# Performance work log

Measured on AMD Instinct MI355X. Metric: run time of the kernel, lower is better.

The kernel has to match this reference:

```python
import jax, jax.numpy as jnp
import numpy as np

B, P, ENC = 128, 196, 2048
D, A, ED, V, L = 512, 512, 512, 10000, 20


def setup_inputs() -> dict:
    key = jax.random.key(0)
    ks = jax.random.split(key, 24)
    s = 0.02
    inp = {
        'encoder_out': jax.random.normal(ks[0], (B, P, ENC), jnp.float32),
        'captions': jax.random.randint(ks[1], (B, L), 0, V),
        'caption_len': jax.random.randint(ks[2], (B,), 2, L + 1).at[0].set(L),
        # embedding (uniform(-0.1, 0.1) per init_weights)
        'emb_w': jax.random.uniform(ks[3], (V, ED), jnp.float32, -0.1, 0.1),
        # LSTMCell: input = ED + ENC, hidden = D, gates order i,f,g,o
        'Wih': jax.random.normal(ks[4], (4 * D, ED + ENC), jnp.float32) * s,
        'Whh': jax.random.normal(ks[5], (4 * D, D), jnp.float32) * s,
        'bih': jax.random.normal(ks[6], (4 * D,), jnp.float32) * s,
        'bhh': jax.random.normal(ks[7], (4 * D,), jnp.float32) * s,
        # init hidden state projections
        'h0_w': jax.random.normal(ks[8], (D, ENC), jnp.float32) * s,
        'h0_b': jnp.zeros((D,), jnp.float32),
        'c0_w': jax.random.normal(ks[9], (D, ENC), jnp.float32) * s,
        'c0_b': jnp.zeros((D,), jnp.float32),
        # gate D -> ENC
        'gate_w': jax.random.normal(ks[10], (ENC, D), jnp.float32) * s,
        'gate_b': jnp.zeros((ENC,), jnp.float32),
        # output projection D -> V (uniform(-0.1,0.1), bias 0 per init_weights)
        'lin_w': jax.random.uniform(ks[11], (V, D), jnp.float32, -0.1, 0.1),
        'lin_b': jnp.zeros((V,), jnp.float32),
        # attention network
        'ea_w': jax.random.normal(ks[12], (A, ENC), jnp.float32) * s,
        'ea_b': jnp.zeros((A,), jnp.float32),
        'da_w': jax.random.normal(ks[13], (A, D), jnp.float32) * s,
        'da_b': jnp.zeros((A,), jnp.float32),
        'fa_w': jax.random.normal(ks[14], (1, A), jnp.float32) * s,
        'fa_b': jnp.zeros((1,), jnp.float32),
    }
    return inp


def reference(encoder_out, captions, caption_len, emb_w, Wih, Whh, bih, bhh,
              h0_w, h0_b, c0_w, c0_b, gate_w, gate_b, lin_w, lin_b,
              ea_w, ea_b, da_w, da_b, fa_w, fa_b):
    # sort by caption length descending (as in torch .sort(descending=True))
    order = jnp.argsort(-caption_len)
    cap_len = caption_len[order]
    enc = encoder_out[order]            # [B, P, ENC]
    caps = captions[order]              # [B, L]
    dec_len = cap_len - 1               # per-example decode lengths

    emb = emb_w[caps]                   # [B, L, ED]
    mean_enc = enc.mean(axis=1)         # [B, ENC]
    h0 = mean_enc @ h0_w.T + h0_b       # [B, D]
    c0 = mean_enc @ c0_w.T + c0_b
    att1 = enc @ ea_w.T + ea_b          # [B, P, A] precomputed encoder attention

    T = caps.shape[1] - 1               # static max decode steps (caption_len[0]=L)

    def step(carry, i):
        h, c = carry
        # Bahdanau attention
        att2 = h @ da_w.T + da_b                                   # [B, A]
        e = (jax.nn.relu(att1 + att2[:, None, :]) @ fa_w.T + fa_b)[..., 0]  # [B, P]
        alpha = jax.nn.softmax(e, axis=1)
        awe = jnp.einsum('bp,bpe->be', alpha, enc)                 # [B, ENC]
        g = jax.nn.sigmoid(h @ gate_w.T + gate_b)
        awe = g * awe
        # LSTMCell
        x = jnp.concatenate([emb[:, i, :], awe], axis=1)           # [B, ED+ENC]
        gates = x @ Wih.T + bih + h @ Whh.T + bhh                  # [B, 4D]
        gi, gf, gg, go = jnp.split(gates, 4, axis=1)
        c_new = jax.nn.sigmoid(gf) * c + jax.nn.sigmoid(gi) * jnp.tanh(gg)
        h_new = jax.nn.sigmoid(go) * jnp.tanh(c_new)
        active = (i < dec_len)[:, None]                            # ragged mask
        # inactive rows keep old state (matches h[:batch_size_i] slicing)
        h2 = jnp.where(active, h_new, h)
        c2 = jnp.where(active, c_new, c)
        # dropout is identity in eval; output projection masked to zeros
        pred = jnp.where(active, h_new @ lin_w.T + lin_b, 0.0)     # [B, V]
        alpha = jnp.where(active, alpha, 0.0)
        return (h2, c2), (pred, alpha)

    (_, _), (preds, alphas) = jax.lax.scan(step, (h0, c0), jnp.arange(T))
    pred = jnp.swapaxes(preds, 0, 1)     # [B, T, V]
    alphas = jnp.swapaxes(alphas, 0, 1)  # [B, T, P]
    return pred, caps, dec_len, alphas, order
```

## Files before the change

kernel.cpp:

```cpp
#include <hip/hip_runtime.h>
#include <hip/hip_bf16.h>
#include <math.h>

#define Bn 128
#define Pn 196
#define ENCn 2048
#define Dn 512
#define An 512
#define EDn 512
#define Vn 10000
#define Ln 20
#define Tn 19

typedef short v8s __attribute__((ext_vector_type(8)));
typedef float v4f __attribute__((ext_vector_type(4)));

__device__ __forceinline__ float sigf(float x){ return 1.f/(1.f+__expf(-x)); }
__device__ __forceinline__ unsigned short f2bf(float f){
  unsigned u = __float_as_uint(f);
  return (unsigned short)((u + 0x7FFFu + ((u>>16)&1u)) >> 16);
}
__device__ __forceinline__ float bf2f(unsigned short h){
  return __uint_as_float(((unsigned)h)<<16);
}


__global__ void k_order(const int* __restrict__ caption_len,
                        const int* __restrict__ captions,
                        int* __restrict__ order_i, int* __restrict__ declen_i,
                        int* __restrict__ caps_s,
                        float* __restrict__ out_caps, float* __restrict__ out_declen,
                        float* __restrict__ out_order)
{
  __shared__ int lens[Bn];
  int b = threadIdx.x;
  lens[b] = caption_len[b];
  __syncthreads();
  int lb = lens[b];
  int r = 0;
  for (int j = 0; j < Bn; ++j) {
    int lj = lens[j];
    r += (int)((lj > lb) || (lj == lb && j < b));
  }
  order_i[r] = b;
  declen_i[r] = lb - 1;
  out_order[r] = (float)b;
  out_declen[r] = (float)(lb - 1);
  for (int t = 0; t < Ln; ++t) {
    int cv = captions[b*Ln + t];
    caps_s[r*Ln + t] = cv;
    out_caps[r*Ln + t] = (float)cv;
  }
}

__global__ void k_setup_bias(const float* __restrict__ bih, const float* __restrict__ bhh,
                             const float* __restrict__ da_b, const float* __restrict__ gate_b,
                             const float* __restrict__ h0_b, const float* __restrict__ c0_b,
                             float* __restrict__ bsum_r, float* __restrict__ dg_b,
                             float* __restrict__ hc_b)
{
  int i = blockIdx.x*256 + threadIdx.x;
  if (i < 2048) {
    int d = i >> 2, g = i & 3;
    bsum_r[i] = bih[g*512+d] + bhh[g*512+d];
  }
  if (i < 2560) dg_b[i] = (i < 512) ? da_b[i] : gate_b[i-512];
  if (i < 1024) hc_b[i] = (i < 512) ? h0_b[i] : c0_b[i-512];
}

__global__ void k_cvt(const float* __restrict__ src, unsigned short* __restrict__ dst, int n)
{
  int i = (blockIdx.x*256 + threadIdx.x)*4;
  if (i < n) {
    float4 v = *(const float4*)(src + i);
    dst[i+0]=f2bf(v.x); dst[i+1]=f2bf(v.y); dst[i+2]=f2bf(v.z); dst[i+3]=f2bf(v.w);
  }
}

__global__ void k_wcat(const float* __restrict__ Wih, const float* __restrict__ Whh,
                       unsigned short* __restrict__ dst)
{
  int i = (blockIdx.x*256 + threadIdx.x)*4;
  if (i >= 2048*3072) return;
  int rp = i/3072, j = i - rp*3072;
  int d = rp >> 2, g = rp & 3;
  int r = g*512 + d;
  const float* s = (j < 2560) ? (Wih + (size_t)r*2560 + j) : (Whh + (size_t)r*512 + (j-2560));
  float4 v = *(const float4*)s;
  dst[i+0]=f2bf(v.x); dst[i+1]=f2bf(v.y); dst[i+2]=f2bf(v.z); dst[i+3]=f2bf(v.w);
}

__global__ void k_cvt_enc(const float* __restrict__ enc, const int* __restrict__ order_i,
                          unsigned short* __restrict__ dst)
{
  int id = blockIdx.x;
  int b = id / Pn, p = id - b*Pn;
  const float* src = enc + ((size_t)order_i[b]*Pn + p)*ENCn;
  unsigned short* d = dst + (size_t)id*ENCn;
  int i = threadIdx.x*8;
  float4 v0 = *(const float4*)(src+i), v1 = *(const float4*)(src+i+4);
  d[i+0]=f2bf(v0.x); d[i+1]=f2bf(v0.y); d[i+2]=f2bf(v0.z); d[i+3]=f2bf(v0.w);
  d[i+4]=f2bf(v1.x); d[i+5]=f2bf(v1.y); d[i+6]=f2bf(v1.z); d[i+7]=f2bf(v1.w);
}

__global__ void k_mean(const unsigned short* __restrict__ enc_bf,
                       unsigned short* __restrict__ mean_bf)
{
  int b = blockIdx.x;
  const unsigned short* eb = enc_bf + (size_t)b*Pn*ENCn;
  for (int e = threadIdx.x; e < ENCn; e += 256) {
    float s = 0.f;
    for (int p = 0; p < Pn; ++p) s += bf2f(eb[(size_t)p*ENCn + e]);
    mean_bf[b*ENCn + e] = f2bf(s * (1.f/196.f));
  }
}

__global__ void k_zero(uint4* __restrict__ p, int n)
{
  int i = blockIdx.x*256 + threadIdx.x;
  if (i < n) p[i] = uint4{0,0,0,0};
}

__global__ void k_emb_all(const int* __restrict__ caps_s, const float* __restrict__ emb_w,
                          unsigned short* __restrict__ xh_all)
{
  int id = blockIdx.x; int t = id >> 7, b = id & 127;
  int tok = caps_s[b*Ln + t];
  const float* src = emb_w + (size_t)tok*EDn;
  unsigned short* d = xh_all + ((size_t)t*Bn + b)*3072;
  int i = threadIdx.x*2;
  float2 v = *(const float2*)(src+i);
  d[i] = f2bf(v.x); d[i+1] = f2bf(v.y);
}

__global__ void k_h2bf(const float* __restrict__ hc, float* __restrict__ c,
                       unsigned short* __restrict__ h_bf, unsigned short* __restrict__ xh_all)
{
  int b = blockIdx.x, d = threadIdx.x;
  float hv = hc[b*1024 + d];
  float cv = hc[b*1024 + 512 + d];
  c[b*Dn + d] = cv;
  unsigned short hb = f2bf(hv);
  h_bf[b*Dn + d] = hb;
  xh_all[(size_t)b*3072 + 2560 + d] = hb;
}

__global__ __launch_bounds__(256) void k_mfma_gemm(
    const unsigned short* __restrict__ Aw, const unsigned short* __restrict__ Bw,
    const float* __restrict__ bias, float* __restrict__ Cp,
    int N, int K, size_t ldc,
    const int* __restrict__ actlen, int t)
{
  __shared__ unsigned short smA[2][4096];
  __shared__ unsigned short smB[2][4096];
  const int tid = threadIdx.x;
  const int bm0 = blockIdx.y*64, bn0 = blockIdx.x*64;
  if (actlen && actlen[bm0] <= t) return;

  const int lane = tid & 63, w = tid >> 6;
  const int wr = w >> 1, wc = w & 1;
  const int lrow = lane & 15, kq = lane >> 4;

  v4f acc[2][2];
  #pragma unroll
  for (int i=0;i<2;++i)
    #pragma unroll
    for (int j=0;j<2;++j) acc[i][j] = (v4f)0.f;

  const int nt = K >> 6;

  auto stage = [&](int buf, int k0) {
    #pragma unroll
    for (int it = 0; it < 2; ++it) {
      int s = it*256 + tid;
      int row = s >> 3;
      int kb  = (s & 7) ^ (row & 7);
      *(v8s*)&smA[buf][s*8] = *(const v8s*)(Aw + (size_t)(bm0+row)*K + k0 + kb*8);
      *(v8s*)&smB[buf][s*8] = *(const v8s*)(Bw + (size_t)(bn0+row)*K + k0 + kb*8);
    }
  };
  auto compute = [&](int buf) {
    #pragma unroll
    for (int kc = 0; kc < 2; ++kc) {
      v8s aF[2], bF[2];
      #pragma unroll
      for (int mi = 0; mi < 2; ++mi) {
        int row = wr*32 + mi*16 + lrow;
        int kb = kc*4 + kq;
        aF[mi] = *(const v8s*)&smA[buf][row*64 + ((kb ^ (row&7))<<3)];
      }
      #pragma unroll
      for (int ni = 0; ni < 2; ++ni) {
        int row = wc*32 + ni*16 + lrow;
        int kb = kc*4 + kq;
        bF[ni] = *(const v8s*)&smB[buf][row*64 + ((kb ^ (row&7))<<3)];
      }
      #pragma unroll
      for (int mi = 0; mi < 2; ++mi)
        #pragma unroll
        for (int ni = 0; ni < 2; ++ni)
          acc[mi][ni] = __builtin_amdgcn_mfma_f32_16x16x32_bf16(aF[mi], bF[ni], acc[mi][ni], 0, 0, 0);
    }
  };

  stage(0, 0);
  __syncthreads();
  for (int tk = 0; tk < nt; ++tk) {
    if (tk + 1 < nt) stage((tk+1)&1, (tk+1)<<6);
    compute(tk&1);
    __syncthreads();
  }

  #pragma unroll
  for (int mi=0; mi<2; ++mi)
    #pragma unroll
    for (int ni=0; ni<2; ++ni)
      #pragma unroll
      for (int r=0; r<4; ++r) {
        int m = bm0 + wr*32 + mi*16 + kq*4 + r;
        int n = bn0 + wc*32 + ni*16 + lrow;
        Cp[(size_t)m*ldc + n] = acc[mi][ni][r] + bias[n];
      }
}

__global__ __launch_bounds__(256) void k_att1(
    const unsigned short* __restrict__ Aw, const unsigned short* __restrict__ Bw,
    const float* __restrict__ bias, unsigned short* __restrict__ Cp)
{
  __shared__ unsigned short smA[2][8192];
  __shared__ unsigned short smB[2][4096];
  const int tid = threadIdx.x;
  const int id = blockIdx.x;
  const int g = (id & 7)*196 + (id >> 3);
  const int bm0 = (g >> 3) * 128, bn0 = (g & 7) * 64;
  const int K = ENCn;

  const int lane = tid & 63, w = tid >> 6;
  const int wr = w >> 1, wc = w & 1;
  const int lrow = lane & 15, kq = lane >> 4;

  v4f acc[4][2];
  #pragma unroll
  for (int i=0;i<4;++i)
    #pragma unroll
    for (int j=0;j<2;++j) acc[i][j] = (v4f)0.f;

  auto stage = [&](int buf, int k0) {
    #pragma unroll
    for (int it = 0; it < 4; ++it) {
      int s = it*256 + tid;
      int row = s >> 3;
      int kb  = (s & 7) ^ (row & 7);
      *(v8s*)&smA[buf][s*8] = *(const v8s*)(Aw + (size_t)(bm0+row)*K + k0 + kb*8);
    }
    #pragma unroll
    for (int it = 0; it < 2; ++it) {
      int s = it*256 + tid;
      int row = s >> 3;
      int kb  = (s & 7) ^ (row & 7);
      *(v8s*)&smB[buf][s*8] = *(const v8s*)(Bw + (size_t)(bn0+row)*K + k0 + kb*8);
    }
  };
  auto compute = [&](int buf) {
    #pragma unroll
    for (int kc = 0; kc < 2; ++kc) {
      v8s aF[4], bF[2];
      #pragma unroll
      for (int mi = 0; mi < 4; ++mi) {
        int row = wr*64 + mi*16 + lrow;
        int kb = kc*4 + kq;
        aF[mi] = *(const v8s*)&smA[buf][row*64 + ((kb ^ (row&7))<<3)];
      }
      #pragma unroll
      for (int ni = 0; ni < 2; ++ni) {
        int row = wc*32 + ni*16 + lrow;
        int kb = kc*4 + kq;
        bF[ni] = *(const v8s*)&smB[buf][row*64 + ((kb ^ (row&7))<<3)];
      }
      #pragma unroll
      for (int mi = 0; mi < 4; ++mi)
        #pragma unroll
        for (int ni = 0; ni < 2; ++ni)
          acc[mi][ni] = __builtin_amdgcn_mfma_f32_16x16x32_bf16(aF[mi], bF[ni], acc[mi][ni], 0, 0, 0);
    }
  };

  stage(0, 0);
  __syncthreads();
  const int nt = K >> 6;
  for (int tk = 0; tk < nt; ++tk) {
    if (tk + 1 < nt) stage((tk+1)&1, (tk+1)<<6);
    compute(tk&1);
    __syncthreads();
  }

  #pragma unroll
  for (int mi=0; mi<4; ++mi)
    #pragma unroll
    for (int ni=0; ni<2; ++ni)
      #pragma unroll
      for (int r=0; r<4; ++r) {
        int m = bm0 + wr*64 + mi*16 + kq*4 + r;
        int n = bn0 + wc*32 + ni*16 + lrow;
        Cp[(size_t)m*An + n] = f2bf(acc[mi][ni][r] + bias[n]);
      }
}

__global__ __launch_bounds__(256) void k_gates_lstm(
    const unsigned short* __restrict__ Aw, const unsigned short* __restrict__ Bw,
    const float* __restrict__ bias,
    float* __restrict__ c, unsigned short* __restrict__ h_bf,
    unsigned short* __restrict__ h_all, unsigned short* __restrict__ xh_all,
    const int* __restrict__ declen_i, int t)
{
  __shared__ unsigned short smA[2][4096];
  __shared__ unsigned short smB[2][4096];
  __shared__ float smC[64][65];
  const int tid = threadIdx.x;
  const int bm0 = blockIdx.y*64, bn0 = blockIdx.x*64;
  if (declen_i[bm0] <= t) return;

  const int lane = tid & 63, w = tid >> 6;
  const int wr = w >> 1, wc = w & 1;
  const int lrow = lane & 15, kq = lane >> 4;
  const int K = 3072;

  v4f acc[2][2];
  #pragma unroll
  for (int i=0;i<2;++i)
    #pragma unroll
    for (int j=0;j<2;++j) acc[i][j] = (v4f)0.f;

  auto stage = [&](int buf, int k0) {
    #pragma unroll
    for (int it = 0; it < 2; ++it) {
      int s = it*256 + tid;
      int row = s >> 3;
      int kb  = (s & 7) ^ (row & 7);
      *(v8s*)&smA[buf][s*8] = *(const v8s*)(Aw + (size_t)(bm0+row)*K + k0 + kb*8);
      *(v8s*)&smB[buf][s*8] = *(const v8s*)(Bw + (size_t)(bn0+row)*K + k0 + kb*8);
    }
  };
  auto compute = [&](int buf) {
    #pragma unroll
    for (int kc = 0; kc < 2; ++kc) {
      v8s aF[2], bF[2];
      #pragma unroll
      for (int mi = 0; mi < 2; ++mi) {
        int row = wr*32 + mi*16 + lrow;
        int kb = kc*4 + kq;
        aF[mi] = *(const v8s*)&smA[buf][row*64 + ((kb ^ (row&7))<<3)];
      }
      #pragma unroll
      for (int ni = 0; ni < 2; ++ni) {
        int row = wc*32 + ni*16 + lrow;
        int kb = kc*4 + kq;
        bF[ni] = *(const v8s*)&smB[buf][row*64 + ((kb ^ (row&7))<<3)];
      }
      #pragma unroll
      for (int mi = 0; mi < 2; ++mi)
        #pragma unroll
        for (int ni = 0; ni < 2; ++ni)
          acc[mi][ni] = __builtin_amdgcn_mfma_f32_16x16x32_bf16(aF[mi], bF[ni], acc[mi][ni], 0, 0, 0);
    }
  };

  stage(0, 0);
  __syncthreads();
  const int nt = K >> 6;
  for (int tk = 0; tk < nt; ++tk) {
    if (tk + 1 < nt) stage((tk+1)&1, (tk+1)<<6);
    compute(tk&1);
    __syncthreads();
  }

  #pragma unroll
  for (int mi=0; mi<2; ++mi)
    #pragma unroll
    for (int ni=0; ni<2; ++ni)
      #pragma unroll
      for (int r=0; r<4; ++r) {
        int ml = wr*32 + mi*16 + kq*4 + r;
        int nl = wc*32 + ni*16 + lrow;
        smC[ml][nl] = acc[mi][ni][r] + bias[bn0 + nl];
      }
  __syncthreads();

  for (int idx = tid; idx < 1024; idx += 256) {
    int ml = idx >> 4, dl = idx & 15;
    int b = bm0 + ml;
    if (t < declen_i[b]) {
      int dg = (bn0 >> 2) + dl;
      float gi = smC[ml][dl*4+0];
      float gf = smC[ml][dl*4+1];
      float gg = smC[ml][dl*4+2];
      float go = smC[ml][dl*4+3];
      float cv = c[b*Dn + dg];
      float cn = sigf(gf)*cv + sigf(gi)*tanhf(gg);
      float hn = sigf(go)*tanhf(cn);
      c[b*Dn + dg] = cn;
      unsigned short hb = f2bf(hn);
      h_bf[b*Dn + dg] = hb;
      h_all[((size_t)t*Bn + b)*Dn + dg] = hb;
      if (t + 1 < Tn)
        xh_all[((size_t)(t+1)*Bn + b)*3072 + 2560 + dg] = hb;
    }
  }
}

__global__ __launch_bounds__(256) void k_pred(
    const unsigned short* __restrict__ Aw, const unsigned short* __restrict__ Bw,
    const float* __restrict__ bias, float* __restrict__ out_pred,
    const int* __restrict__ declen_i)
{
  __shared__ unsigned short smA[2][4096];
  __shared__ unsigned short smB[2][4096];
  const int tid = threadIdx.x;
  const int bm0 = blockIdx.y*64, bn0 = blockIdx.x*64;
  const int t0 = bm0 >> 7, b0 = bm0 & 127;

  if (declen_i[b0] <= t0) {
    for (int i = tid; i < 4096; i += 256) {
      int ml = i >> 6, nl = i & 63;
      int n = bn0 + nl;
      if (n < Vn) {
        int m = bm0 + ml;
        out_pred[((size_t)(m & 127)*Tn + (m >> 7))*Vn + n] = 0.f;
      }
    }
    return;
  }

  const int lane = tid & 63, w = tid >> 6;
  const int wr = w >> 1, wc = w & 1;
  const int lrow = lane & 15, kq = lane >> 4;
  const int K = 512;

  v4f acc[2][2];
  #pragma unroll
  for (int i=0;i<2;++i)
    #pragma unroll
    for (int j=0;j<2;++j) acc[i][j] = (v4f)0.f;

  auto stage = [&](int buf, int k0) {
    #pragma unroll
    for (int it = 0; it < 2; ++it) {
      int s = it*256 + tid;
      int row = s >> 3;
      int kb  = (s & 7) ^ (row & 7);
      *(v8s*)&smA[buf][s*8] = *(const v8s*)(Aw + (size_t)(bm0+row)*K + k0 + kb*8);
      {
        int gn = bn0 + row; if (gn >= Vn) gn = Vn-1;
        *(v8s*)&smB[buf][s*8] = *(const v8s*)(Bw + (size_t)gn*K + k0 + kb*8);
      }
    }
  };
  auto compute = [&](int buf) {
    #pragma unroll
    for (int kc = 0; kc < 2; ++kc) {
      v8s aF[2], bF[2];
      #pragma unroll
      for (int mi = 0; mi < 2; ++mi) {
        int row = wr*32 + mi*16 + lrow;
        int kb = kc*4 + kq;
        aF[mi] = *(const v8s*)&smA[buf][row*64 + ((kb ^ (row&7))<<3)];
      }
      #pragma unroll
      for (int ni = 0; ni < 2; ++ni) {
        int row = wc*32 + ni*16 + lrow;
        int kb = kc*4 + kq;
        bF[ni] = *(const v8s*)&smB[buf][row*64 + ((kb ^ (row&7))<<3)];
      }
      #pragma unroll
      for (int mi = 0; mi < 2; ++mi)
        #pragma unroll
        for (int ni = 0; ni < 2; ++ni)
          acc[mi][ni] = __builtin_amdgcn_mfma_f32_16x16x32_bf16(aF[mi], bF[ni], acc[mi][ni], 0, 0, 0);
    }
  };

  stage(0, 0);
  __syncthreads();
  const int nt = K >> 6;
  for (int tk = 0; tk < nt; ++tk) {
    if (tk + 1 < nt) stage((tk+1)&1, (tk+1)<<6);
    compute(tk&1);
    __syncthreads();
  }

  #pragma unroll
  for (int mi=0; mi<2; ++mi)
    #pragma unroll
    for (int ni=0; ni<2; ++ni)
      #pragma unroll
      for (int r=0; r<4; ++r) {
        int m = bm0 + wr*32 + mi*16 + kq*4 + r;
        int n = bn0 + wc*32 + ni*16 + lrow;
        if (n < Vn) {
          int b = m & 127, tt = m >> 7;
          float v = (tt < declen_i[b]) ? (acc[mi][ni][r] + bias[n]) : 0.f;
          out_pred[((size_t)b*Tn + tt)*Vn + n] = v;
        }
      }
}

__global__ __launch_bounds__(256) void k_esm(
    const unsigned short* __restrict__ att1, const float* __restrict__ att2g,
    const float* __restrict__ fa_w, const float* __restrict__ fa_b,
    float* __restrict__ alpha, float* __restrict__ out_alph,
    const int* __restrict__ declen_i, int t)
{
  int b = blockIdx.x;
  int tid = threadIdx.x;
  if (t >= declen_i[b]) {
    if (tid < Pn)
      out_alph[(size_t)b*Tn*Pn + (size_t)t*Pn + tid] = 0.f;
    return;
  }
  __shared__ float a2s[An];
  __shared__ float fws[An];
  __shared__ float es[Pn];
  __shared__ float wred[4];
  __shared__ float wsum[4];
  for (int i = tid; i < An; i += 256) { a2s[i] = att2g[(size_t)b*2560 + i]; fws[i] = fa_w[i]; }
  __syncthreads();
  int lane = tid & 63, w = tid >> 6;
  if (tid < Pn) {
    const unsigned short* row = att1 + ((size_t)b*Pn + tid)*An;
    float s = 0.f;
    #pragma unroll 4
    for (int kb = 0; kb < 64; ++kb) {
      const v8s vv = *(const v8s*)(row + kb*8);
      #pragma unroll
      for (int j = 0; j < 8; ++j) {
        int a = kb*8 + j;
        float v = bf2f((unsigned short)vv[j]) + a2s[a];
        s += fmaxf(v, 0.f) * fws[a];
      }
    }
    es[tid] = s + fa_b[0];
  }
  __syncthreads();
  float m = -1e30f;
  for (int p = tid; p < Pn; p += 256) m = fmaxf(m, es[p]);
  for (int off = 32; off; off >>= 1) m = fmaxf(m, __shfl_down(m, off));
  if (lane == 0) wred[w] = m;
  __syncthreads();
  m = fmaxf(fmaxf(wred[0], wred[1]), fmaxf(wred[2], wred[3]));
  float s = 0.f;
  for (int p = tid; p < Pn; p += 256) { float ev = __expf(es[p] - m); es[p] = ev; s += ev; }
  for (int off = 32; off; off >>= 1) s += __shfl_down(s, off);
  if (lane == 0) wsum[w] = s;
  __syncthreads();
  s = wsum[0] + wsum[1] + wsum[2] + wsum[3];
  float inv = 1.f / s;
  for (int p = tid; p < Pn; p += 256) {
    float al = es[p] * inv;
    alpha[b*Pn + p] = al;
    out_alph[(size_t)b*Tn*Pn + (size_t)t*Pn + p] = al;
  }
}

__global__ __launch_bounds__(256) void k_awe_gate(
    const unsigned short* __restrict__ enc_bf,
    const float* __restrict__ alpha, const float* __restrict__ att2g,
    unsigned short* __restrict__ xh_t, const int* __restrict__ declen_i, int t)
{
  int b = blockIdx.y;
  if (t >= declen_i[b]) return;
  __shared__ float als[Pn];
  __shared__ float red[8][256];
  int tid = threadIdx.x;
  if (tid < Pn) als[tid] = alpha[b*Pn + tid];
  __syncthreads();
  int e0 = blockIdx.x*256;
  int ec = tid & 31, ps = tid >> 5;
  const unsigned short* eb = enc_bf + (size_t)b*Pn*ENCn + e0 + ec*8;
  float s[8] = {};
  for (int p = ps; p < Pn; p += 8) {
    v8s v = *(const v8s*)(eb + (size_t)p*ENCn);
    float a = als[p];
    #pragma unroll
    for (int j = 0; j < 8; ++j) s[j] += a * bf2f((unsigned short)v[j]);
  }
  #pragma unroll
  for (int j = 0; j < 8; ++j) red[ps][ec*8+j] = s[j];
  __syncthreads();
  {
    int e = tid;
    float tsum = 0.f;
    #pragma unroll
    for (int k = 0; k < 8; ++k) tsum += red[k][e];
    int eg = e0 + e;
    float g = sigf(att2g[(size_t)b*2560 + 512 + eg]);
    xh_t[(size_t)b*3072 + 512 + eg] = f2bf(g*tsum);
  }
}


extern "C" void kernel_launch(void* const* d_in, const int* in_sizes, int n_in,
                              void* d_out, int out_size, void* d_ws, size_t ws_size,
                              hipStream_t stream)
{
  const float* enc     = (const float*)d_in[0];
  const int*   captions= (const int*)d_in[1];
  const int*   cap_len = (const int*)d_in[2];
  const float* emb_w   = (const float*)d_in[3];
  const float* Wih     = (const float*)d_in[4];
  const float* Whh     = (const float*)d_in[5];
  const float* bih     = (const float*)d_in[6];
  const float* bhh     = (const float*)d_in[7];
  const float* h0_w    = (const float*)d_in[8];
  const float* h0_b    = (const float*)d_in[9];
  const float* c0_w    = (const float*)d_in[10];
  const float* c0_b    = (const float*)d_in[11];
  const float* gate_w  = (const float*)d_in[12];
  const float* gate_b  = (const float*)d_in[13];
  const float* lin_w   = (const float*)d_in[14];
  const float* lin_b   = (const float*)d_in[15];
  const float* ea_w    = (const float*)d_in[16];
  const float* ea_b    = (const float*)d_in[17];
  const float* da_w    = (const float*)d_in[18];
  const float* da_b    = (const float*)d_in[19];
  const float* fa_w    = (const float*)d_in[20];
  const float* fa_b    = (const float*)d_in[21];

  float* out = (float*)d_out;
  float* out_pred   = out;
  float* out_caps   = out + (size_t)Bn*Tn*Vn;
  float* out_declen = out_caps + Bn*Ln;
  float* out_alph   = out_declen + Bn;
  float* out_order  = out_alph + (size_t)Bn*Tn*Pn;

  char* wp = (char*)d_ws;
  auto alloc = [&](size_t bytes)->void* {
    void* p = (void*)wp; wp += (bytes + 255) & ~(size_t)255; return p;
  };
  int*   order_i  = (int*)alloc(Bn*4);
  int*   declen_i = (int*)alloc(Bn*4);
  int*   caps_s   = (int*)alloc(Bn*Ln*4);
  unsigned short* enc_bf  = (unsigned short*)alloc((size_t)Bn*Pn*ENCn*2);
  unsigned short* mean_bf = (unsigned short*)alloc((size_t)Bn*ENCn*2);
  float* hc       = (float*)alloc((size_t)Bn*1024*4);
  float* c        = (float*)alloc((size_t)Bn*Dn*4);
  unsigned short* h_bf   = (unsigned short*)alloc((size_t)Bn*Dn*2);
  unsigned short* h_all  = (unsigned short*)alloc((size_t)Tn*Bn*Dn*2);
  unsigned short* xh_all = (unsigned short*)alloc((size_t)Tn*Bn*3072*2);
  unsigned short* att1   = (unsigned short*)alloc((size_t)Bn*Pn*An*2);
  float* att2g    = (float*)alloc((size_t)Bn*2560*4);
  float* alpha    = (float*)alloc((size_t)Bn*Pn*4);
  unsigned short* ea_bf   = (unsigned short*)alloc((size_t)An*ENCn*2);
  unsigned short* lin_bf  = (unsigned short*)alloc((size_t)Vn*Dn*2);
  unsigned short* h0c0_bf = (unsigned short*)alloc((size_t)1024*ENCn*2);
  unsigned short* dg_bf   = (unsigned short*)alloc((size_t)2560*Dn*2);
  unsigned short* wcat_bf = (unsigned short*)alloc((size_t)2048*3072*2);
  float* bsum = (float*)alloc(2048*4);
  float* dg_b = (float*)alloc(2560*4);
  float* hc_b = (float*)alloc(1024*4);

  k_order<<<1,128,0,stream>>>(cap_len, captions, order_i, declen_i, caps_s,
                              out_caps, out_declen, out_order);
  k_setup_bias<<<10,256,0,stream>>>(bih, bhh, da_b, gate_b, h0_b, c0_b, bsum, dg_b, hc_b);
  k_cvt<<<(An*ENCn/4+255)/256,256,0,stream>>>(ea_w, ea_bf, An*ENCn);
  k_cvt<<<(Vn*Dn/4+255)/256,256,0,stream>>>(lin_w, lin_bf, Vn*Dn);
  k_cvt<<<(Dn*ENCn/4+255)/256,256,0,stream>>>(h0_w, h0c0_bf, Dn*ENCn);
  k_cvt<<<(Dn*ENCn/4+255)/256,256,0,stream>>>(c0_w, h0c0_bf + (size_t)512*ENCn, Dn*ENCn);
  k_cvt<<<(An*Dn/4+255)/256,256,0,stream>>>(da_w, dg_bf, An*Dn);
  k_cvt<<<(ENCn*Dn/4+255)/256,256,0,stream>>>(gate_w, dg_bf + (size_t)512*Dn, ENCn*Dn);
  k_wcat<<<(2048*3072/4+255)/256,256,0,stream>>>(Wih, Whh, wcat_bf);
  k_cvt_enc<<<Bn*Pn,256,0,stream>>>(enc, order_i, enc_bf);
  k_mean<<<Bn,256,0,stream>>>(enc_bf, mean_bf);
  k_zero<<<((int)((size_t)Tn*Bn*3072*2/16)+255)/256,256,0,stream>>>(
      (uint4*)xh_all, (int)((size_t)Tn*Bn*3072*2/16));
  k_emb_all<<<Tn*Bn,256,0,stream>>>(caps_s, emb_w, xh_all);

  k_mfma_gemm<<<dim3(16,2),256,0,stream>>>(
      mean_bf, h0c0_bf, hc_b, hc, 1024, ENCn, 1024, nullptr, 0);
  k_h2bf<<<Bn,512,0,stream>>>(hc, c, h_bf, xh_all);

  k_att1<<<dim3(196*8),256,0,stream>>>(enc_bf, ea_bf, ea_b, att1);

  for (int t = 0; t < Tn; ++t) {
    unsigned short* xh_t = xh_all + (size_t)t*Bn*3072;
    k_mfma_gemm<<<dim3(40,2),256,0,stream>>>(
        h_bf, dg_bf, dg_b, att2g, 2560, Dn, 2560, declen_i, t);
    k_esm<<<Bn,256,0,stream>>>(att1, att2g, fa_w, fa_b, alpha, out_alph, declen_i, t);
    k_awe_gate<<<dim3(8,Bn),256,0,stream>>>(enc_bf, alpha, att2g, xh_t, declen_i, t);
    k_gates_lstm<<<dim3(32,2),256,0,stream>>>(
        xh_t, wcat_bf, bsum, c, h_bf, h_all, xh_all, declen_i, t);
  }

  k_pred<<<dim3((Vn+63)/64, (Tn*Bn)/64),256,0,stream>>>(
      h_all, lin_bf, lin_b, out_pred, declen_i);
}
```

Before: 1.639 ms.

## Fuse weight conversion kernels, drop xh zero-fill, widen pred GEMM tile to 128 rows

Merges six float-to-bf16 weight conversion launches into one kernel that picks its source from a cumulative offset. Removes the zero-fill of the xh_all buffer. Changes the output projection GEMM to 128x64 tiles, one per timestep, which doubles reuse of each B (lin_w) tile. The cost is that the early-out for fully inactive blocks is gone, so masked rows are now computed too. Dropping the zero-fill assumes every xh_all element read later is written elsewhere, and that may not hold.

```diff
diff --git a/kernel.cpp b/kernel.cpp
--- a/kernel.cpp
+++ b/kernel.cpp
@@ -68,13 +68,35 @@
   if (i < 1024) hc_b[i] = (i < 512) ? h0_b[i] : c0_b[i-512];
 }
 
-__global__ void k_cvt(const float* __restrict__ src, unsigned short* __restrict__ dst, int n)
+#define C_EA  (512*2048)
+#define C_LIN (10000*512)
+#define C_H0  (512*2048)
+#define C_C0  (512*2048)
+#define C_DA  (512*512)
+#define C_GW  (2048*512)
+#define CUM1  (C_EA)
+#define CUM2  (CUM1 + C_LIN)
+#define CUM3  (CUM2 + C_H0)
+#define CUM4  (CUM3 + C_C0)
+#define CUM5  (CUM4 + C_DA)
+#define CUM6  (CUM5 + C_GW)
+
+__global__ void k_cvt6(const float* __restrict__ ea_w, const float* __restrict__ lin_w,
+                       const float* __restrict__ h0_w, const float* __restrict__ c0_w,
+                       const float* __restrict__ da_w, const float* __restrict__ gate_w,
+                       unsigned short* __restrict__ ea_bf, unsigned short* __restrict__ lin_bf,
+                       unsigned short* __restrict__ h0c0_bf, unsigned short* __restrict__ dg_bf)
 {
   int i = (blockIdx.x*256 + threadIdx.x)*4;
-  if (i < n) {
-    float4 v = *(const float4*)(src + i);
-    dst[i+0]=f2bf(v.x); dst[i+1]=f2bf(v.y); dst[i+2]=f2bf(v.z); dst[i+3]=f2bf(v.w);
-  }
+  const float* src; unsigned short* dst; int off;
+  if      (i < CUM1) { src = ea_w;   dst = ea_bf;                    off = i; }
+  else if (i < CUM2) { src = lin_w;  dst = lin_bf;                   off = i - CUM1; }
+  else if (i < CUM3) { src = h0_w;   dst = h0c0_bf;                  off = i - CUM2; }
+  else if (i < CUM4) { src = c0_w;   dst = h0c0_bf + (size_t)C_H0;   off = i - CUM3; }
+  else if (i < CUM5) { src = da_w;   dst = dg_bf;                    off = i - CUM4; }
+  else               { src = gate_w; dst = dg_bf + (size_t)C_DA;     off = i - CUM5; }
+  float4 v = *(const float4*)(src + off);
+  dst[off+0]=f2bf(v.x); dst[off+1]=f2bf(v.y); dst[off+2]=f2bf(v.z); dst[off+3]=f2bf(v.w);
 }
 
 __global__ void k_wcat(const float* __restrict__ Wih, const float* __restrict__ Whh,
@@ -113,12 +135,6 @@
     for (int p = 0; p < Pn; ++p) s += bf2f(eb[(size_t)p*ENCn + e]);
     mean_bf[b*ENCn + e] = f2bf(s * (1.f/196.f));
   }
-}
-
-__global__ void k_zero(uint4* __restrict__ p, int n)
-{
-  int i = blockIdx.x*256 + threadIdx.x;
-  if (i < n) p[i] = uint4{0,0,0,0};
 }
 
 __global__ void k_emb_all(const int* __restrict__ caps_s, const float* __restrict__ emb_w,
@@ -413,55 +429,47 @@
     const float* __restrict__ bias, float* __restrict__ out_pred,
     const int* __restrict__ declen_i)
 {
-  __shared__ unsigned short smA[2][4096];
+  __shared__ unsigned short smA[2][8192];
   __shared__ unsigned short smB[2][4096];
   const int tid = threadIdx.x;
-  const int bm0 = blockIdx.y*64, bn0 = blockIdx.x*64;
-  const int t0 = bm0 >> 7, b0 = bm0 & 127;
-
-  if (declen_i[b0] <= t0) {
-    for (int i = tid; i < 4096; i += 256) {
-      int ml = i >> 6, nl = i & 63;
-      int n = bn0 + nl;
-      if (n < Vn) {
-        int m = bm0 + ml;
-        out_pred[((size_t)(m & 127)*Tn + (m >> 7))*Vn + n] = 0.f;
-      }
-    }
-    return;
-  }
+  const int t0 = blockIdx.y;
+  const int bm0 = t0*128, bn0 = blockIdx.x*64;
+  const int K = Dn;
 
   const int lane = tid & 63, w = tid >> 6;
   const int wr = w >> 1, wc = w & 1;
   const int lrow = lane & 15, kq = lane >> 4;
-  const int K = 512;
-
-  v4f acc[2][2];
-  #pragma unroll
-  for (int i=0;i<2;++i)
+
+  v4f acc[4][2];
+  #pragma unroll
+  for (int i=0;i<4;++i)
     #pragma unroll
     for (int j=0;j<2;++j) acc[i][j] = (v4f)0.f;
 
   auto stage = [&](int buf, int k0) {
+    #pragma unroll
+    for (int it = 0; it < 4; ++it) {
+      int s = it*256 + tid;
+      int row = s >> 3;
+      int kb  = (s & 7) ^ (row & 7);
+      *(v8s*)&smA[buf][s*8] = *(const v8s*)(Aw + (size_t)(bm0+row)*K + k0 + kb*8);
+    }
     #pragma unroll
     for (int it = 0; it < 2; ++it) {
       int s = it*256 + tid;
       int row = s >> 3;
       int kb  = (s & 7) ^ (row & 7);
-      *(v8s*)&smA[buf][s*8] = *(const v8s*)(Aw + (size_t)(bm0+row)*K + k0 + kb*8);
-      {
-        int gn = bn0 + row; if (gn >= Vn) gn = Vn-1;
-        *(v8s*)&smB[buf][s*8] = *(const v8s*)(Bw + (size_t)gn*K + k0 + kb*8);
-      }
+      int gn = bn0 + row; if (gn >= Vn) gn = Vn-1;
+      *(v8s*)&smB[buf][s*8] = *(const v8s*)(Bw + (size_t)gn*K + k0 + kb*8);
     }
   };
   auto compute = [&](int buf) {
     #pragma unroll
     for (int kc = 0; kc < 2; ++kc) {
-      v8s aF[2], bF[2];
-      #pragma unroll
-      for (int mi = 0; mi < 2; ++mi) {
-        int row = wr*32 + mi*16 + lrow;
+      v8s aF[4], bF[2];
+      #pragma unroll
+      for (int mi = 0; mi < 4; ++mi) {
+        int row = wr*64 + mi*16 + lrow;
         int kb = kc*4 + kq;
         aF[mi] = *(const v8s*)&smA[buf][row*64 + ((kb ^ (row&7))<<3)];
       }
@@ -472,7 +480,7 @@
         bF[ni] = *(const v8s*)&smB[buf][row*64 + ((kb ^ (row&7))<<3)];
       }
       #pragma unroll
-      for (int mi = 0; mi < 2; ++mi)
+      for (int mi = 0; mi < 4; ++mi)
         #pragma unroll
         for (int ni = 0; ni < 2; ++ni)
           acc[mi][ni] = __builtin_amdgcn_mfma_f32_16x16x32_bf16(aF[mi], bF[ni], acc[mi][ni], 0, 0, 0);
@@ -489,17 +497,16 @@
   }
 
   #pragma unroll
-  for (int mi=0; mi<2; ++mi)
+  for (int mi=0; mi<4; ++mi)
     #pragma unroll
     for (int ni=0; ni<2; ++ni)
       #pragma unroll
       for (int r=0; r<4; ++r) {
-        int m = bm0 + wr*32 + mi*16 + kq*4 + r;
+        int b = wr*64 + mi*16 + kq*4 + r;
         int n = bn0 + wc*32 + ni*16 + lrow;
         if (n < Vn) {
-          int b = m & 127, tt = m >> 7;
-          float v = (tt < declen_i[b]) ? (acc[mi][ni][r] + bias[n]) : 0.f;
-          out_pred[((size_t)b*Tn + tt)*Vn + n] = v;
+          float v = (t0 < declen_i[b]) ? (acc[mi][ni][r] + bias[n]) : 0.f;
+          out_pred[((size_t)b*Tn + t0)*Vn + n] = v;
         }
       }
 }
@@ -661,17 +668,11 @@
   k_order<<<1,128,0,stream>>>(cap_len, captions, order_i, declen_i, caps_s,
                               out_caps, out_declen, out_order);
   k_setup_bias<<<10,256,0,stream>>>(bih, bhh, da_b, gate_b, h0_b, c0_b, bsum, dg_b, hc_b);
-  k_cvt<<<(An*ENCn/4+255)/256,256,0,stream>>>(ea_w, ea_bf, An*ENCn);
-  k_cvt<<<(Vn*Dn/4+255)/256,256,0,stream>>>(lin_w, lin_bf, Vn*Dn);
-  k_cvt<<<(Dn*ENCn/4+255)/256,256,0,stream>>>(h0_w, h0c0_bf, Dn*ENCn);
-  k_cvt<<<(Dn*ENCn/4+255)/256,256,0,stream>>>(c0_w, h0c0_bf + (size_t)512*ENCn, Dn*ENCn);
-  k_cvt<<<(An*Dn/4+255)/256,256,0,stream>>>(da_w, dg_bf, An*Dn);
-  k_cvt<<<(ENCn*Dn/4+255)/256,256,0,stream>>>(gate_w, dg_bf + (size_t)512*Dn, ENCn*Dn);
+  k_cvt6<<<9352,256,0,stream>>>(ea_w, lin_w, h0_w, c0_w, da_w, gate_w,
+                                ea_bf, lin_bf, h0c0_bf, dg_bf);
   k_wcat<<<(2048*3072/4+255)/256,256,0,stream>>>(Wih, Whh, wcat_bf);
   k_cvt_enc<<<Bn*Pn,256,0,stream>>>(enc, order_i, enc_bf);
   k_mean<<<Bn,256,0,stream>>>(enc_bf, mean_bf);
-  k_zero<<<((int)((size_t)Tn*Bn*3072*2/16)+255)/256,256,0,stream>>>(
-      (uint4*)xh_all, (int)((size_t)Tn*Bn*3072*2/16));
   k_emb_all<<<Tn*Bn,256,0,stream>>>(caps_s, emb_w, xh_all);
 
   k_mfma_gemm<<<dim3(16,2),256,0,stream>>>(
@@ -690,6 +691,6 @@
         xh_t, wcat_bf, bsum, c, h_bf, h_all, xh_all, declen_i, t);
   }
 
-  k_pred<<<dim3((Vn+63)/64, (Tn*Bn)/64),256,0,stream>>>(
+  k_pred<<<dim3((Vn+63)/64, Tn),256,0,stream>>>(
       h_all, lin_bf, lin_b, out_pred, declen_i);
 }
```

New measurement: 1.703 ms. 1.04x slower.
